# Optimization experiments

Measured on AMD Instinct MI355X. Metric: run time of the kernel, lower is better.

The kernel has to match this reference:

```python
import jax, jax.numpy as jnp
import numpy as np

B, S, D = 2, 2048, 768
H, STRIDE = 12, 8
HD = D // H  # 64


def setup_inputs() -> dict:
    key = jax.random.key(0)
    k0, k1, k2 = jax.random.split(key, 3)
    x = jax.random.normal(k0, (B, S, D), dtype=jnp.float32)
    qkv_w = jax.random.normal(k1, (3 * D, D), dtype=jnp.float32) * 0.02
    qkv_b = jnp.zeros((3 * D,), dtype=jnp.float32)
    out_w = jax.random.normal(k2, (D, D), dtype=jnp.float32) * 0.02
    out_b = jnp.zeros((D,), dtype=jnp.float32)
    return {"x": x, "qkv_w": qkv_w, "qkv_b": qkv_b, "out_w": out_w, "out_b": out_b}


def _stride_mask(S, stride, causal):
    i = jnp.arange(S)[:, None]
    j = jnp.arange(S)[None, :]
    strided = (j % stride == 0)
    if causal:
        strided = strided & (j <= i)
    # diagonal always attended; previous token attended for i > 0
    return strided | (j == i) | (j == i - 1)


def reference(x, qkv_w, qkv_b, out_w, out_b):
    Bx, Sx, Dx = x.shape
    qkv = x @ qkv_w.T + qkv_b                      # [B,S,3D]
    qkv = qkv.reshape(Bx, Sx, 3, H, HD)
    q, k, v = jnp.transpose(qkv, (2, 0, 3, 1, 4))  # each [B,H,S,HD]
    scale = HD ** -0.5
    attn = jnp.einsum('bhid,bhjd->bhij', q, k) * scale  # [B,H,S,S]
    mask = _stride_mask(Sx, STRIDE, True)          # [S,S] bool
    attn = jnp.where(mask[None, None], attn, -jnp.inf)
    a = jax.nn.softmax(attn, axis=-1)
    # every row has at least the diagonal unmasked, so no NaN rows;
    # nan_to_num kept for exact parity with the torch module
    a = jnp.nan_to_num(a, nan=0.0)
    out = jnp.einsum('bhij,bhjd->bhid', a, v)      # [B,H,S,HD]
    out = jnp.transpose(out, (0, 2, 1, 3)).reshape(Bx, Sx, Dx)
    return out @ out_w.T + out_b
```

## Files before the change

### kernel.cpp

```cpp
#include <hip/hip_runtime.h>
#include <hip/hip_bf16.h>
#include <stdint.h>

#define H_   12
#define S_   2048
#define D_   768
#define HD_  64
#define MS_  256

typedef __bf16 bf16_8 __attribute__((ext_vector_type(8)));
typedef float  f32_4  __attribute__((ext_vector_type(4)));

typedef __attribute__((address_space(1))) void* gas_ptr;
typedef __attribute__((address_space(3))) void* las_ptr;

__device__ __forceinline__ void g2l16(const void* g, void* l) {
  __builtin_amdgcn_global_load_lds((gas_ptr)g, (las_ptr)l, 16, 0, 0);
}

__device__ __forceinline__ f32_4 mfma16(bf16_8 a, bf16_8 b, f32_4 c) {
  return __builtin_amdgcn_mfma_f32_16x16x32_bf16(a, b, c, 0, 0, 0);
}

__device__ __forceinline__ bf16_8 ld8(const __hip_bfloat16* p) {
  return *reinterpret_cast<const bf16_8*>(p);
}

__global__ __launch_bounds__(256) void cvt3_f32_bf16(
    const float* __restrict__ a, const float* __restrict__ b,
    const float* __restrict__ c, __hip_bfloat16* __restrict__ out,
    int na4, int nb4) {
  const int t = blockIdx.x * 256 + threadIdx.x;
  float4 f;
  if (t < na4)            f = reinterpret_cast<const float4*>(a)[t];
  else if (t < na4 + nb4) f = reinterpret_cast<const float4*>(b)[t - na4];
  else                    f = reinterpret_cast<const float4*>(c)[t - na4 - nb4];
  union { __hip_bfloat16 h[4]; ushort4 u; } p;
  p.h[0] = __float2bfloat16(f.x);
  p.h[1] = __float2bfloat16(f.y);
  p.h[2] = __float2bfloat16(f.z);
  p.h[3] = __float2bfloat16(f.w);
  reinterpret_cast<ushort4*>(out)[t] = p.u;
}

template <int MODE, int BN>
__global__ __launch_bounds__(256, 4) void gemm_bt(
    const __hip_bfloat16* __restrict__ A, const __hip_bfloat16* __restrict__ B,
    const float* __restrict__ bias,
    __hip_bfloat16* __restrict__ O0, __hip_bfloat16* __restrict__ O1,
    __hip_bfloat16* __restrict__ O2, __hip_bfloat16* __restrict__ O3,
    __hip_bfloat16* __restrict__ O4, float* __restrict__ OF,
    int M, int N, int K) {
  constexpr int NTJ  = BN / 32;
  constexpr int HB   = BN * 32;
  constexpr int DB   = (MODE == 1) ? 2 : 1;
  constexpr int ABUF = 64 * 64;
  constexpr int BBUF = BN * 64;
  __shared__ __bf16 sA[DB * ABUF];
  __shared__ __bf16 sB[DB * BBUF];
  const int tid  = threadIdx.x;
  const int lane = tid & 63;
  const int wv   = tid >> 6;

  const int nwg  = gridDim.x * gridDim.y;
  const int hw   = blockIdx.y * gridDim.x + blockIdx.x;
  const int swz  = (hw & 7) * (nwg >> 3) + (hw >> 3);
  const int bx   = swz % gridDim.x;
  const int by   = swz / gridDim.x;

  const int m0 = by * 64;
  const int n0 = bx * BN;
  const int wr = (wv >> 1) * 32;
  const int wc = (wv & 1) * (BN / 2);

  f32_4 acc[2][NTJ] = {};

  const __hip_bfloat16* aS = A + (size_t)(m0 + (tid >> 2)) * K + ((tid & 3) << 3);
  const __hip_bfloat16* bS = B + (size_t)(n0 + (tid >> 2)) * K + ((tid & 3) << 3);
  const size_t half = (size_t)64 * K;
  __bf16* dA = &sA[tid * 8];
  __bf16* dB = &sB[tid * 8];

  const int fr = lane & 15;
  const int kq = (lane >> 4) << 3;

  auto stage = [&](int k0, int buf) {
    const __hip_bfloat16* a = aS + k0;
    const __hip_bfloat16* b = bS + k0;
    __bf16* da = dA + buf * ABUF;
    __bf16* db = dB + buf * BBUF;
    g2l16(a,      da);
    g2l16(a + 32, da + 2048);
    g2l16(b,      db);
    if constexpr (BN == 128) {
      g2l16(b + half,      db + 2048);
      g2l16(b + 32,        db + 4096);
      g2l16(b + half + 32, db + 4096 + 2048);
    } else {
      g2l16(b + 32, db + 2048);
    }
  };

  auto compute = [&](const __bf16* bA, const __bf16* bB) {
#pragma unroll
    for (int kk = 0; kk < 2; ++kk) {
      bf16_8 af[2], bfm[NTJ];
#pragma unroll
      for (int t = 0; t < 2; ++t)
        af[t] = *reinterpret_cast<const bf16_8*>(
            &bA[kk * 2048 + (wr + t * 16 + fr) * 32 + kq]);
#pragma unroll
      for (int t = 0; t < NTJ; ++t)
        bfm[t] = *reinterpret_cast<const bf16_8*>(
            &bB[kk * HB + (wc + t * 16 + fr) * 32 + kq]);
#pragma unroll
      for (int ti = 0; ti < 2; ++ti)
#pragma unroll
        for (int tj = 0; tj < NTJ; ++tj)
          acc[ti][tj] = mfma16(af[ti], bfm[tj], acc[ti][tj]);
    }
  };

  if constexpr (DB == 1) {
    for (int k0 = 0; k0 < K; k0 += 64) {
      stage(k0, 0);
      __syncthreads();
      compute(sA, sB);
      __syncthreads();
    }
  } else {
    stage(0, 0);
    __syncthreads();
    int cur = 0;
    for (int k0 = 0; k0 < K; k0 += 64) {
      if (k0 + 64 < K) stage(k0 + 64, cur ^ 1);
      compute(&sA[cur * ABUF], &sB[cur * BBUF]);
      __syncthreads();
      cur ^= 1;
    }
  }

  const int crow = (lane >> 4) << 2;
  const int ccol = lane & 15;
#pragma unroll
  for (int ti = 0; ti < 2; ++ti) {
    const int gmb = m0 + wr + ti * 16 + crow;
#pragma unroll
    for (int tj = 0; tj < NTJ; ++tj) {
      const int gn = n0 + wc + tj * 16 + ccol;
      const float bv = bias[gn];
      if (MODE == 0) {
        const int t   = gn / D_;
        const int rem = gn - t * D_;
        const int hh = rem >> 6, dd = rem & 63;
        __hip_bfloat16* dst = (t == 0) ? O0 : (t == 1) ? O1 : O2;
#pragma unroll
        for (int r = 0; r < 4; ++r) {
          const int gm = gmb + r;
          const int bb = gm >> 11, ss = gm & (S_ - 1);
          const __hip_bfloat16 hv = __float2bfloat16(acc[ti][tj][r] + bv);
          dst[(((size_t)(bb * H_ + hh) << 11) + ss) * HD_ + dd] = hv;
          if (r == 0 && (gmb & 7) == 0) {
            if (t == 1)
              O4[(((size_t)(bb * H_ + hh)) * MS_ + (ss >> 3)) * HD_ + dd] = hv;
            else if (t == 2)
              O3[((size_t)(bb * H_ + hh) * HD_ + dd) * MS_ + (ss >> 3)] = hv;
          }
        }
      } else {
#pragma unroll
        for (int r = 0; r < 4; ++r)
          OF[(size_t)(gmb + r) * D_ + gn] = acc[ti][tj][r] + bv;
      }
    }
  }
}

__global__ __launch_bounds__(256) void attn_mfma(
    const __hip_bfloat16* __restrict__ Q, const __hip_bfloat16* __restrict__ Kb,
    const __hip_bfloat16* __restrict__ Ks, const __hip_bfloat16* __restrict__ Vr,
    const __hip_bfloat16* __restrict__ VsT, __hip_bfloat16* __restrict__ ctx) {
  __shared__ __bf16 pt[4][16 * 40];
  __shared__ float ox[3][64][20];
  const int lane = threadIdx.x & 63;
  const int part = threadIdx.x >> 6;
  const int nwg  = gridDim.x;
  const int hw   = blockIdx.x;
  const int task = (hw & 7) * (nwg >> 3) + (hw >> 3);
  const int bh   = task >> 7;
  const int i0   = (task & 127) << 4;
  const int lr   = lane & 15;
  const int quad = lane >> 4;
  const float SC = 0.125f * 1.44269504088896340736f;

  const __hip_bfloat16* Kh  = Kb  + ((size_t)bh << 11) * HD_;
  const __hip_bfloat16* Ksh = Ks  + (size_t)bh * MS_ * HD_;
  const __hip_bfloat16* Vrh = Vr  + ((size_t)bh << 11) * HD_;
  const __hip_bfloat16* Vsh = VsT + (size_t)bh * HD_ * MS_;
  __bf16* ptw = pt[part];

  const int jbase = (i0 >= 8) ? (i0 - 8) : 0;

  bf16_8 vfb[4], kb_[2][2];
  if (part == 3) {
    const __bf16* Vrb = reinterpret_cast<const __bf16*>(Vrh);
#pragma unroll
    for (int ct = 0; ct < 4; ++ct)
#pragma unroll
      for (int e = 0; e < 8; ++e) {
        const int j  = jbase + quad * 8 + e;
        const int jr = (j < S_) ? j : (S_ - 1);
        vfb[ct][e] = Vrb[(size_t)jr * HD_ + ct * 16 + lr];
      }
#pragma unroll
    for (int t = 0; t < 2; ++t) {
      const int j  = jbase + t * 16 + lr;
      const int jr = (j < S_) ? j : (S_ - 1);
      const __hip_bfloat16* kp = Kh + (size_t)jr * HD_ + quad * 8;
      kb_[t][0] = ld8(kp);
      kb_[t][1] = ld8(kp + 32);
    }
  }

  const __hip_bfloat16* qp = Q + (((size_t)bh << 11) + i0 + lr) * HD_ + quad * 8;
  const bf16_8 qf0 = ld8(qp);
  const bf16_8 qf1 = ld8(qp + 32);

  const __bf16 one = (__bf16)1.0f;
  const bf16_8 onesf = {one, one, one, one, one, one, one, one};

  f32_4 Lacc = {}, oacc[4];
#pragma unroll
  for (int ct = 0; ct < 4; ++ct) oacc[ct] = f32_4{0.f, 0.f, 0.f, 0.f};

  const int mmax = (i0 + 15) >> 3;
  const int nstr = (mmax >> 5) + 1;

  auto load_str = [&](int c, bf16_8 (&kf)[2][2], bf16_8 (&vf)[4]) {
    const int mb = c << 5;
#pragma unroll
    for (int t = 0; t < 2; ++t) {
      const __hip_bfloat16* kp = Ksh + (size_t)(mb + t * 16 + lr) * HD_ + quad * 8;
      kf[t][0] = ld8(kp);
      kf[t][1] = ld8(kp + 32);
    }
#pragma unroll
    for (int ct = 0; ct < 4; ++ct)
      vf[ct] = ld8(Vsh + (size_t)(ct * 16 + lr) * MS_ + mb + quad * 8);
  };

  auto softmax_pv = [&](f32_4& s0, f32_4& s1, const bf16_8 (&vf)[4]) {
#pragma unroll
    for (int r = 0; r < 4; ++r) {
      const int row = quad * 4 + r;
      ptw[row * 40 + lr]      = (__bf16)__float2bfloat16(s0[r]);
      ptw[row * 40 + 16 + lr] = (__bf16)__float2bfloat16(s1[r]);
    }
    const bf16_8 pf = *reinterpret_cast<const bf16_8*>(&ptw[lr * 40 + quad * 8]);
#pragma unroll
    for (int ct = 0; ct < 4; ++ct) oacc[ct] = mfma16(pf, vf[ct], oacc[ct]);
    Lacc = mfma16(pf, onesf, Lacc);
  };

  bf16_8 kf[2][2], vf[4], kf2[2][2], vf2[4];
  if (part < nstr) load_str(part, kf, vf);
  for (int c = part; c < nstr; c += 4) {
    const bool more = (c + 4 < nstr);
    if (more) load_str(c + 4, kf2, vf2);
    const int mb = c << 5;

    f32_4 s0 = {}, s1 = {};
    s0 = mfma16(qf0, kf[0][0], s0);
    s0 = mfma16(qf1, kf[0][1], s0);
    s1 = mfma16(qf0, kf[1][0], s1);
    s1 = mfma16(qf1, kf[1][1], s1);

#pragma unroll
    for (int r = 0; r < 4; ++r) {
      const int i = i0 + quad * 4 + r;
      const bool v0 = ((mb + lr) << 3) <= i;
      const bool v1 = ((mb + 16 + lr) << 3) <= i;
      s0[r] = v0 ? exp2f(fminf(s0[r] * SC, 63.f)) : 0.f;
      s1[r] = v1 ? exp2f(fminf(s1[r] * SC, 63.f)) : 0.f;
    }
    softmax_pv(s0, s1, vf);

    if (more) {
#pragma unroll
      for (int t = 0; t < 2; ++t) { kf[t][0] = kf2[t][0]; kf[t][1] = kf2[t][1]; }
#pragma unroll
      for (int ct = 0; ct < 4; ++ct) vf[ct] = vf2[ct];
    }
  }

  if (part == 3) {
    f32_4 s0 = {}, s1 = {};
    s0 = mfma16(qf0, kb_[0][0], s0);
    s0 = mfma16(qf1, kb_[0][1], s0);
    s1 = mfma16(qf0, kb_[1][0], s1);
    s1 = mfma16(qf1, kb_[1][1], s1);

#pragma unroll
    for (int r = 0; r < 4; ++r) {
      const int i = i0 + quad * 4 + r;
      const int j0 = jbase + lr, j1 = jbase + 16 + lr;
      const bool v0 = (j0 == i || j0 == i - 1) && (j0 & 7);
      const bool v1 = (j1 == i || j1 == i - 1) && (j1 & 7);
      s0[r] = v0 ? exp2f(fminf(s0[r] * SC, 63.f)) : 0.f;
      s1[r] = v1 ? exp2f(fminf(s1[r] * SC, 63.f)) : 0.f;
    }
    softmax_pv(s0, s1, vfb);
  }

  if (part) {
#pragma unroll
    for (int ct = 0; ct < 4; ++ct)
#pragma unroll
      for (int r = 0; r < 4; ++r) ox[part - 1][lane][ct * 4 + r] = oacc[ct][r];
#pragma unroll
    for (int r = 0; r < 4; ++r) ox[part - 1][lane][16 + r] = Lacc[r];
  }
  __syncthreads();

  if (!part) {
#pragma unroll
    for (int p = 0; p < 3; ++p) {
#pragma unroll
      for (int ct = 0; ct < 4; ++ct)
#pragma unroll
        for (int r = 0; r < 4; ++r) oacc[ct][r] += ox[p][lane][ct * 4 + r];
#pragma unroll
      for (int r = 0; r < 4; ++r) Lacc[r] += ox[p][lane][16 + r];
    }

    const int b = bh / H_;
    const int h = bh - b * H_;
    f32_4 inv;
#pragma unroll
    for (int r = 0; r < 4; ++r) inv[r] = 1.f / Lacc[r];
#pragma unroll
    for (int r = 0; r < 4; ++r) {
      const int i = i0 + quad * 4 + r;
      __hip_bfloat16* cp = ctx + ((size_t)(b * S_ + i)) * D_ + h * HD_ + lr;
#pragma unroll
      for (int ct = 0; ct < 4; ++ct)
        cp[ct * 16] = __float2bfloat16(oacc[ct][r] * inv[r]);
    }
  }
}

extern "C" void kernel_launch(void* const* d_in, const int* in_sizes, int n_in,
                              void* d_out, int out_size, void* d_ws, size_t ws_size,
                              hipStream_t stream) {
  const float* x    = (const float*)d_in[0];
  const float* qkvw = (const float*)d_in[1];
  const float* qkvb = (const float*)d_in[2];
  const float* outw = (const float*)d_in[3];
  const float* outb = (const float*)d_in[4];
  float* out = (float*)d_out;

  const size_t NX  = (size_t)2 * S_ * D_;
  const size_t NW1 = (size_t)3 * D_ * D_;
  const size_t NW2 = (size_t)D_ * D_;
  const size_t NVS = (size_t)2 * H_ * HD_ * MS_;

  __hip_bfloat16* xb  = (__hip_bfloat16*)d_ws;
  __hip_bfloat16* w1b = xb + NX;
  __hip_bfloat16* w2b = w1b + NW1;
  __hip_bfloat16* q   = w2b + NW2;
  __hip_bfloat16* k   = q + NX;
  __hip_bfloat16* vr  = k + NX;
  __hip_bfloat16* vst = vr + NX;
  __hip_bfloat16* ks  = vst + NVS;
  __hip_bfloat16* ctx = ks + NVS;

  const int na4 = (int)(NX / 4), nb4 = (int)(NW1 / 4), nc4 = (int)(NW2 / 4);
  cvt3_f32_bf16<<<dim3((na4 + nb4 + nc4) / 256), 256, 0, stream>>>(
      x, qkvw, outw, xb, na4, nb4);

  gemm_bt<0, 128><<<dim3(2304 / 128, 4096 / 64), 256, 0, stream>>>(
      xb, w1b, qkvb, q, k, vr, vst, ks, nullptr, 4096, 2304, 768);

  attn_mfma<<<dim3(2 * H_ * S_ / 16), 256, 0, stream>>>(
      q, k, ks, vr, vst, ctx);

  gemm_bt<1, 64><<<dim3(768 / 64, 4096 / 64), 256, 0, stream>>>(
      ctx, w2b, outb, nullptr, nullptr, nullptr, nullptr, nullptr,
      out, 4096, 768, 768);
}
```

Baseline: 138.2 us.

## Process 32 query rows per attention block to reuse strided K/V loads

Each attention workgroup now handles two 16-row query tiles instead of one, halving the grid size. Every strided K/V fragment loaded from global memory is applied to both query tiles, and the local-band (diagonal/previous token) work is split between two waves, one per tile. This is meant to cut redundant K/V global traffic and per-block overhead, at the cost of more registers and shared memory per block and fewer blocks to spread across CUs.

```diff
diff --git a/kernel.cpp b/kernel.cpp
--- a/kernel.cpp
+++ b/kernel.cpp
@@ -180,15 +180,15 @@
     const __hip_bfloat16* __restrict__ Q, const __hip_bfloat16* __restrict__ Kb,
     const __hip_bfloat16* __restrict__ Ks, const __hip_bfloat16* __restrict__ Vr,
     const __hip_bfloat16* __restrict__ VsT, __hip_bfloat16* __restrict__ ctx) {
-  __shared__ __bf16 pt[4][16 * 40];
-  __shared__ float ox[3][64][20];
+  __shared__ __bf16 pt[4][32 * 40];
+  __shared__ float ox[3][64][40];
   const int lane = threadIdx.x & 63;
   const int part = threadIdx.x >> 6;
   const int nwg  = gridDim.x;
   const int hw   = blockIdx.x;
   const int task = (hw & 7) * (nwg >> 3) + (hw >> 3);
-  const int bh   = task >> 7;
-  const int i0   = (task & 127) << 4;
+  const int bh   = task >> 6;
+  const int i0   = (task & 63) << 5;
   const int lr   = lane & 15;
   const int quad = lane >> 4;
   const float SC = 0.125f * 1.44269504088896340736f;
@@ -199,22 +199,22 @@
   const __hip_bfloat16* Vsh = VsT + (size_t)bh * HD_ * MS_;
   __bf16* ptw = pt[part];
 
-  const int jbase = (i0 >= 8) ? (i0 - 8) : 0;
-
   bf16_8 vfb[4], kb_[2][2];
-  if (part == 3) {
+  int jb = 0;
+  if (part >= 2) {
+    jb = (part == 3) ? ((i0 >= 8) ? i0 - 8 : 0) : (i0 + 8);
     const __bf16* Vrb = reinterpret_cast<const __bf16*>(Vrh);
 #pragma unroll
     for (int ct = 0; ct < 4; ++ct)
 #pragma unroll
       for (int e = 0; e < 8; ++e) {
-        const int j  = jbase + quad * 8 + e;
+        const int j  = jb + quad * 8 + e;
         const int jr = (j < S_) ? j : (S_ - 1);
         vfb[ct][e] = Vrb[(size_t)jr * HD_ + ct * 16 + lr];
       }
 #pragma unroll
     for (int t = 0; t < 2; ++t) {
-      const int j  = jbase + t * 16 + lr;
+      const int j  = jb + t * 16 + lr;
       const int jr = (j < S_) ? j : (S_ - 1);
       const __hip_bfloat16* kp = Kh + (size_t)jr * HD_ + quad * 8;
       kb_[t][0] = ld8(kp);
@@ -222,18 +222,21 @@
     }
   }
 
-  const __hip_bfloat16* qp = Q + (((size_t)bh << 11) + i0 + lr) * HD_ + quad * 8;
-  const bf16_8 qf0 = ld8(qp);
-  const bf16_8 qf1 = ld8(qp + 32);
+  const __hip_bfloat16* qpA = Q + (((size_t)bh << 11) + i0 + lr) * HD_ + quad * 8;
+  const bf16_8 qa0 = ld8(qpA);
+  const bf16_8 qa1 = ld8(qpA + 32);
+  const __hip_bfloat16* qpB = qpA + (size_t)16 * HD_;
+  const bf16_8 qb0 = ld8(qpB);
+  const bf16_8 qb1 = ld8(qpB + 32);
 
   const __bf16 one = (__bf16)1.0f;
   const bf16_8 onesf = {one, one, one, one, one, one, one, one};
 
-  f32_4 Lacc = {}, oacc[4];
-#pragma unroll
-  for (int ct = 0; ct < 4; ++ct) oacc[ct] = f32_4{0.f, 0.f, 0.f, 0.f};
-
-  const int mmax = (i0 + 15) >> 3;
+  f32_4 LA = {}, LB = {}, oA[4], oB[4];
+#pragma unroll
+  for (int ct = 0; ct < 4; ++ct) { oA[ct] = f32_4{0.f,0.f,0.f,0.f}; oB[ct] = f32_4{0.f,0.f,0.f,0.f}; }
+
+  const int mmax = (i0 + 31) >> 3;
   const int nstr = (mmax >> 5) + 1;
 
   auto load_str = [&](int c, bf16_8 (&kf)[2][2], bf16_8 (&vf)[4]) {
@@ -249,17 +252,18 @@
       vf[ct] = ld8(Vsh + (size_t)(ct * 16 + lr) * MS_ + mb + quad * 8);
   };
 
-  auto softmax_pv = [&](f32_4& s0, f32_4& s1, const bf16_8 (&vf)[4]) {
+  auto softmax_pv = [&](int ro, f32_4& s0, f32_4& s1, const bf16_8 (&vf)[4],
+                        f32_4 (&oac)[4], f32_4& La) {
 #pragma unroll
     for (int r = 0; r < 4; ++r) {
-      const int row = quad * 4 + r;
+      const int row = ro + quad * 4 + r;
       ptw[row * 40 + lr]      = (__bf16)__float2bfloat16(s0[r]);
       ptw[row * 40 + 16 + lr] = (__bf16)__float2bfloat16(s1[r]);
     }
-    const bf16_8 pf = *reinterpret_cast<const bf16_8*>(&ptw[lr * 40 + quad * 8]);
-#pragma unroll
-    for (int ct = 0; ct < 4; ++ct) oacc[ct] = mfma16(pf, vf[ct], oacc[ct]);
-    Lacc = mfma16(pf, onesf, Lacc);
+    const bf16_8 pf = *reinterpret_cast<const bf16_8*>(&ptw[(ro + lr) * 40 + quad * 8]);
+#pragma unroll
+    for (int ct = 0; ct < 4; ++ct) oac[ct] = mfma16(pf, vf[ct], oac[ct]);
+    La = mfma16(pf, onesf, La);
   };
 
   bf16_8 kf[2][2], vf[4], kf2[2][2], vf2[4];
@@ -269,56 +273,94 @@
     if (more) load_str(c + 4, kf2, vf2);
     const int mb = c << 5;
 
+    {
+      f32_4 s0 = {}, s1 = {};
+      s0 = mfma16(qa0, kf[0][0], s0);
+      s0 = mfma16(qa1, kf[0][1], s0);
+      s1 = mfma16(qa0, kf[1][0], s1);
+      s1 = mfma16(qa1, kf[1][1], s1);
+#pragma unroll
+      for (int r = 0; r < 4; ++r) {
+        const int i = i0 + quad * 4 + r;
+        const bool v0 = ((mb + lr) << 3) <= i;
+        const bool v1 = ((mb + 16 + lr) << 3) <= i;
+        s0[r] = v0 ? exp2f(fminf(s0[r] * SC, 63.f)) : 0.f;
+        s1[r] = v1 ? exp2f(fminf(s1[r] * SC, 63.f)) : 0.f;
+      }
+      softmax_pv(0, s0, s1, vf, oA, LA);
+    }
+    {
+      f32_4 s0 = {}, s1 = {};
+      s0 = mfma16(qb0, kf[0][0], s0);
+      s0 = mfma16(qb1, kf[0][1], s0);
+      s1 = mfma16(qb0, kf[1][0], s1);
+      s1 = mfma16(qb1, kf[1][1], s1);
+#pragma unroll
+      for (int r = 0; r < 4; ++r) {
+        const int i = i0 + 16 + quad * 4 + r;
+        const bool v0 = ((mb + lr) << 3) <= i;
+        const bool v1 = ((mb + 16 + lr) << 3) <= i;
+        s0[r] = v0 ? exp2f(fminf(s0[r] * SC, 63.f)) : 0.f;
+        s1[r] = v1 ? exp2f(fminf(s1[r] * SC, 63.f)) : 0.f;
+      }
+      softmax_pv(16, s0, s1, vf, oB, LB);
+    }
+
+    if (more) {
+#pragma unroll
+      for (int t = 0; t < 2; ++t) { kf[t][0] = kf2[t][0]; kf[t][1] = kf2[t][1]; }
+#pragma unroll
+      for (int ct = 0; ct < 4; ++ct) vf[ct] = vf2[ct];
+    }
+  }
+
+  if (part == 3) {
     f32_4 s0 = {}, s1 = {};
-    s0 = mfma16(qf0, kf[0][0], s0);
-    s0 = mfma16(qf1, kf[0][1], s0);
-    s1 = mfma16(qf0, kf[1][0], s1);
-    s1 = mfma16(qf1, kf[1][1], s1);
-
+    s0 = mfma16(qa0, kb_[0][0], s0);
+    s0 = mfma16(qa1, kb_[0][1], s0);
+    s1 = mfma16(qa0, kb_[1][0], s1);
+    s1 = mfma16(qa1, kb_[1][1], s1);
 #pragma unroll
     for (int r = 0; r < 4; ++r) {
       const int i = i0 + quad * 4 + r;
-      const bool v0 = ((mb + lr) << 3) <= i;
-      const bool v1 = ((mb + 16 + lr) << 3) <= i;
-      s0[r] = v0 ? exp2f(fminf(s0[r] * SC, 63.f)) : 0.f;
-      s1[r] = v1 ? exp2f(fminf(s1[r] * SC, 63.f)) : 0.f;
-    }
-    softmax_pv(s0, s1, vf);
-
-    if (more) {
-#pragma unroll
-      for (int t = 0; t < 2; ++t) { kf[t][0] = kf2[t][0]; kf[t][1] = kf2[t][1]; }
-#pragma unroll
-      for (int ct = 0; ct < 4; ++ct) vf[ct] = vf2[ct];
-    }
-  }
-
-  if (part == 3) {
-    f32_4 s0 = {}, s1 = {};
-    s0 = mfma16(qf0, kb_[0][0], s0);
-    s0 = mfma16(qf1, kb_[0][1], s0);
-    s1 = mfma16(qf0, kb_[1][0], s1);
-    s1 = mfma16(qf1, kb_[1][1], s1);
-
-#pragma unroll
-    for (int r = 0; r < 4; ++r) {
-      const int i = i0 + quad * 4 + r;
-      const int j0 = jbase + lr, j1 = jbase + 16 + lr;
+      const int j0 = jb + lr, j1 = jb + 16 + lr;
       const bool v0 = (j0 == i || j0 == i - 1) && (j0 & 7);
       const bool v1 = (j1 == i || j1 == i - 1) && (j1 & 7);
       s0[r] = v0 ? exp2f(fminf(s0[r] * SC, 63.f)) : 0.f;
       s1[r] = v1 ? exp2f(fminf(s1[r] * SC, 63.f)) : 0.f;
     }
-    softmax_pv(s0, s1, vfb);
+    softmax_pv(0, s0, s1, vfb, oA, LA);
+  } else if (part == 2) {
+    f32_4 s0 = {}, s1 = {};
+    s0 = mfma16(qb0, kb_[0][0], s0);
+    s0 = mfma16(qb1, kb_[0][1], s0);
+    s1 = mfma16(qb0, kb_[1][0], s1);
+    s1 = mfma16(qb1, kb_[1][1], s1);
+#pragma unroll
+    for (int r = 0; r < 4; ++r) {
+      const int i = i0 + 16 + quad * 4 + r;
+      const int j0 = jb + lr, j1 = jb + 16 + lr;
+      const bool v0 = (j0 == i || j0 == i - 1) && (j0 & 7);
+      const bool v1 = (j1 == i || j1 == i - 1) && (j1 & 7);
+      s0[r] = v0 ? exp2f(fminf(s0[r] * SC, 63.f)) : 0.f;
+      s1[r] = v1 ? exp2f(fminf(s1[r] * SC, 63.f)) : 0.f;
+    }
+    softmax_pv(16, s0, s1, vfb, oB, LB);
   }
 
   if (part) {
 #pragma unroll
     for (int ct = 0; ct < 4; ++ct)
 #pragma unroll
-      for (int r = 0; r < 4; ++r) ox[part - 1][lane][ct * 4 + r] = oacc[ct][r];
-#pragma unroll
-    for (int r = 0; r < 4; ++r) ox[part - 1][lane][16 + r] = Lacc[r];
+      for (int r = 0; r < 4; ++r) {
+        ox[part - 1][lane][ct * 4 + r]      = oA[ct][r];
+        ox[part - 1][lane][20 + ct * 4 + r] = oB[ct][r];
+      }
+#pragma unroll
+    for (int r = 0; r < 4; ++r) {
+      ox[part - 1][lane][16 + r] = LA[r];
+      ox[part - 1][lane][36 + r] = LB[r];
+    }
   }
   __syncthreads();
 
@@ -328,23 +370,34 @@
 #pragma unroll
       for (int ct = 0; ct < 4; ++ct)
 #pragma unroll
-        for (int r = 0; r < 4; ++r) oacc[ct][r] += ox[p][lane][ct * 4 + r];
-#pragma unroll
-      for (int r = 0; r < 4; ++r) Lacc[r] += ox[p][lane][16 + r];
+        for (int r = 0; r < 4; ++r) {
+          oA[ct][r] += ox[p][lane][ct * 4 + r];
+          oB[ct][r] += ox[p][lane][20 + ct * 4 + r];
+        }
+#pragma unroll
+      for (int r = 0; r < 4; ++r) {
+        LA[r] += ox[p][lane][16 + r];
+        LB[r] += ox[p][lane][36 + r];
+      }
     }
 
     const int b = bh / H_;
     const int h = bh - b * H_;
-    f32_4 inv;
-#pragma unroll
-    for (int r = 0; r < 4; ++r) inv[r] = 1.f / Lacc[r];
+    f32_4 invA, invB;
+#pragma unroll
+    for (int r = 0; r < 4; ++r) { invA[r] = 1.f / LA[r]; invB[r] = 1.f / LB[r]; }
 #pragma unroll
     for (int r = 0; r < 4; ++r) {
-      const int i = i0 + quad * 4 + r;
-      __hip_bfloat16* cp = ctx + ((size_t)(b * S_ + i)) * D_ + h * HD_ + lr;
+      const int iA = i0 + quad * 4 + r;
+      __hip_bfloat16* cpA = ctx + ((size_t)(b * S_ + iA)) * D_ + h * HD_ + lr;
 #pragma unroll
       for (int ct = 0; ct < 4; ++ct)
-        cp[ct * 16] = __float2bfloat16(oacc[ct][r] * inv[r]);
+        cpA[ct * 16] = __float2bfloat16(oA[ct][r] * invA[r]);
+      const int iB = iA + 16;
+      __hip_bfloat16* cpB = ctx + ((size_t)(b * S_ + iB)) * D_ + h * HD_ + lr;
+#pragma unroll
+      for (int ct = 0; ct < 4; ++ct)
+        cpB[ct * 16] = __float2bfloat16(oB[ct][r] * invB[r]);
     }
   }
 }
@@ -381,7 +434,7 @@
   gemm_bt<0, 128><<<dim3(2304 / 128, 4096 / 64), 256, 0, stream>>>(
       xb, w1b, qkvb, q, k, vr, vst, ks, nullptr, 4096, 2304, 768);
 
-  attn_mfma<<<dim3(2 * H_ * S_ / 16), 256, 0, stream>>>(
+  attn_mfma<<<dim3(2 * H_ * S_ / 32), 256, 0, stream>>>(
       q, k, ks, vr, vst, ctx);
 
   gemm_bt<1, 64><<<dim3(768 / 64, 4096 / 64), 256, 0, stream>>>(
```

Result: faster. 134.7 us (-2.5%).
